# Kernel tuning notes

Hardware: AMD Instinct MI355X
Metric: run time of the kernel (lower is better)

The kernel has to match this reference:

```python
import jax, jax.numpy as jnp
import numpy as np

D_MODEL = 1024
NUM_HEADS = 16
D_HEAD = D_MODEL // NUM_HEADS
NEG_INF = float(np.finfo(np.float32).min)


def setup_inputs() -> dict:
    key = jax.random.key(0)
    ks = jax.random.split(key, 6)
    B, S = 2, 2048
    q = jax.random.normal(ks[0], (B, S, D_MODEL), dtype=jnp.float32)
    k = jax.random.normal(ks[1], (B, S, D_MODEL), dtype=jnp.float32)
    v = jax.random.normal(ks[2], (B, S, D_MODEL), dtype=jnp.float32)
    # causal boolean mask: True = attend
    attn_mask = jnp.tril(jnp.ones((S, S), dtype=bool))
    # nn.Linear(d_model, d_model, bias=False) weights: [out, in]; y = x @ W.T
    init_scale = 1.0 / np.sqrt(D_MODEL)
    Wq = jax.random.uniform(ks[3], (D_MODEL, D_MODEL), jnp.float32, -init_scale, init_scale)
    Wk = jax.random.uniform(ks[4], (D_MODEL, D_MODEL), jnp.float32, -init_scale, init_scale)
    Wv = jax.random.uniform(ks[5], (D_MODEL, D_MODEL), jnp.float32, -init_scale, init_scale)
    return {"query": q, "key": k, "value": v, "Wq": Wq, "Wk": Wk, "Wv": Wv,
            "attn_mask": attn_mask}


def _split_heads(x):
    # [B, S, D_MODEL] -> [B, H, S, d_head]
    B, S, _ = x.shape
    return x.reshape(B, S, NUM_HEADS, D_HEAD).transpose(0, 2, 1, 3)


def reference(query, key, value, Wq, Wk, Wv, attn_mask):
    B, Sq, _ = query.shape
    Sk = key.shape[1]
    q = _split_heads(query @ Wq.T)   # [B, H, Sq, dh]
    k = _split_heads(key @ Wk.T)     # [B, H, Sk, dh]
    v = _split_heads(value @ Wv.T)   # [B, H, Sk, dh]
    scale = 1.0 / np.sqrt(D_HEAD)
    scores = jnp.einsum('bhqd,bhkd->bhqk', q, k) * scale  # [B, H, Sq, Sk]
    scores = jnp.where(attn_mask[None, None, :, :], scores, NEG_INF)
    attn_weights = jax.nn.softmax(scores, axis=-1)
    ctx = jnp.einsum('bhqk,bhkd->bhqd', attn_weights, v)   # [B, H, Sq, dh]
    context = ctx.transpose(0, 2, 1, 3).reshape(B, Sq, D_MODEL)
    return context, attn_weights
```

## Files before the change

### kernel.cpp

```cpp
#include <hip/hip_runtime.h>
#include <hip/hip_bf16.h>

#define B_ 2
#define H_ 16
#define S_ 2048
#define DH_ 64
#define DM_ 1024
#define BH_ (B_*H_)
#define CTX_ELEMS (B_*S_*DM_)
#define ATTNW_ELEMS ((size_t)BH_*S_*S_)
#define HEAD_ELEMS (S_*DH_)

typedef __attribute__((ext_vector_type(4))) float  f32x4;
typedef __attribute__((ext_vector_type(8))) short  short8;
typedef __attribute__((ext_vector_type(4))) unsigned short ush4;
typedef unsigned short u16;
typedef unsigned int u32;

__device__ __forceinline__ u16 f2bf(float f) {
  union { __hip_bfloat16 h; u16 u; } cv;
  cv.h = __float2bfloat16(f);
  return cv.u;
}
__device__ __forceinline__ float bf2f(u16 u) {
  union { unsigned int i; float f; } cv;
  cv.i = ((unsigned int)u) << 16;
  return cv.f;
}

__device__ __forceinline__ void gload_lds16(const u16* g, u16* l) {
  __builtin_amdgcn_global_load_lds(
      (const __attribute__((address_space(1))) u32*)g,
      (__attribute__((address_space(3))) u32*)l, 16, 0, 0);
}

__global__ __launch_bounds__(256) void convert_all(
    const float* __restrict__ q, const float* __restrict__ k, const float* __restrict__ v,
    const float* __restrict__ wq, const float* __restrict__ wk, const float* __restrict__ wv,
    u16* __restrict__ xb, u16* __restrict__ wb)
{
  const int t = blockIdx.y;
  const float* s; u16* d; int nblk;
  if (t < 3) {
    s = (t == 0) ? wq : (t == 1) ? wk : wv;
    d = wb + (size_t)t * (DM_ * DM_);
    nblk = 512;
  } else {
    s = (t == 3) ? q : (t == 4) ? k : v;
    d = xb + (size_t)(t - 3) * ((size_t)B_ * S_ * DM_);
    nblk = 2048;
  }
  if (blockIdx.x >= nblk) return;
  const int i = (blockIdx.x * 256 + threadIdx.x) * 8;
  f32x4 a = *(const f32x4*)(s + i);
  f32x4 b = *(const f32x4*)(s + i + 4);
  short8 p;
#pragma unroll
  for (int j = 0; j < 4; ++j) { p[j] = (short)f2bf(a[j]); p[4 + j] = (short)f2bf(b[j]); }
  *(short8*)(d + i) = p;
}

__global__ __launch_bounds__(256) void proj_gemm(
    const u16* __restrict__ Xb, const u16* __restrict__ Wb,
    u16* __restrict__ O0, u16* __restrict__ O1, u16* __restrict__ O2)
{
  u16* O = (blockIdx.z == 0) ? O0 : (blockIdx.z == 1) ? O1 : O2;
  const u16* A = Xb + (size_t)blockIdx.z * ((size_t)B_ * S_ * DM_);
  const u16* W = Wb + (size_t)blockIdx.z * (DM_ * DM_);

  const int m0 = blockIdx.x * 128;
  const int n0 = blockIdx.y * 128;

  __shared__ u16 As[128 * 32];
  __shared__ u16 Bs[128 * 32];

  const int tid  = threadIdx.x;
  const int lane = tid & 63;
  const int w    = tid >> 6;
  const int wr   = w >> 1, wc = w & 1;
  const int l15  = lane & 15, l4 = lane >> 4;

  f32x4 acc[4][4];
#pragma unroll
  for (int i = 0; i < 4; ++i)
#pragma unroll
    for (int j = 0; j < 4; ++j) acc[i][j] = (f32x4){0.f, 0.f, 0.f, 0.f};

  const int srow = lane >> 2;
  const int scol = (lane & 3) * 8;
  const int ca = w * 2;
  const u16* ga0 = A + (size_t)(m0 + ca * 16 + srow) * DM_ + scol;
  const u16* ga1 = A + (size_t)(m0 + ca * 16 + 16 + srow) * DM_ + scol;
  const u16* gb0 = W + (size_t)(n0 + ca * 16 + srow) * DM_ + scol;
  const u16* gb1 = W + (size_t)(n0 + ca * 16 + 16 + srow) * DM_ + scol;

  for (int kb = 0; kb < DM_ / 32; ++kb) {
    const int k0 = kb * 32;
    gload_lds16(ga0 + k0, &As[ca * 512]);
    gload_lds16(ga1 + k0, &As[ca * 512 + 512]);
    gload_lds16(gb0 + k0, &Bs[ca * 512]);
    gload_lds16(gb1 + k0, &Bs[ca * 512 + 512]);
    __syncthreads();
    short8 af[4], bfr[4];
#pragma unroll
    for (int i = 0; i < 4; ++i)
      af[i] = *(const short8*)&As[(wr * 64 + i * 16 + l15) * 32 + l4 * 8];
#pragma unroll
    for (int j = 0; j < 4; ++j)
      bfr[j] = *(const short8*)&Bs[(wc * 64 + j * 16 + l15) * 32 + l4 * 8];
#pragma unroll
    for (int i = 0; i < 4; ++i)
#pragma unroll
      for (int j = 0; j < 4; ++j)
        acc[i][j] = __builtin_amdgcn_mfma_f32_16x16x32_bf16(af[i], bfr[j], acc[i][j], 0, 0, 0);
    __syncthreads();
  }

#pragma unroll
  for (int i = 0; i < 4; ++i) {
#pragma unroll
    for (int j = 0; j < 4; ++j) {
#pragma unroll
      for (int r = 0; r < 4; ++r) {
        const int grow = m0 + wr * 64 + i * 16 + l4 * 4 + r;
        const int gcol = n0 + wc * 64 + j * 16 + l15;
        const int b = grow >> 11, s = grow & (S_ - 1);
        const int h = gcol >> 6,  d = gcol & (DH_ - 1);
        O[(size_t)((b << 4) + h) * HEAD_ELEMS + (size_t)s * DH_ + d] = f2bf(acc[i][j][r]);
      }
    }
  }
}

__global__ __launch_bounds__(256) void transpose_v(const u16* __restrict__ vb,
                                                   u16* __restrict__ vt)
{
  __shared__ u16 T[64][72];
  const int bh = blockIdx.y;
  const int s0 = blockIdx.x * 64;
  const int tid = threadIdx.x;
  {
    const int sl = tid >> 2, dof = (tid & 3) * 16;
    const u16* src = vb + (size_t)bh * HEAD_ELEMS + (size_t)(s0 + sl) * DH_ + dof;
    *(short8*)&T[sl][dof]     = *(const short8*)(src);
    *(short8*)&T[sl][dof + 8] = *(const short8*)(src + 8);
  }
  __syncthreads();
  {
    const int dd = tid >> 2, sof = (tid & 3) * 16;
    u16* dst = vt + (size_t)bh * HEAD_ELEMS + (size_t)dd * S_ + s0 + sof;
    short8 t0, t1;
#pragma unroll
    for (int j = 0; j < 8; ++j) t0[j] = (short)T[sof + j][dd];
#pragma unroll
    for (int j = 0; j < 8; ++j) t1[j] = (short)T[sof + 8 + j][dd];
    *(short8*)(dst)     = t0;
    *(short8*)(dst + 8) = t1;
  }
}

#define PROW 2048
#define ATT_SMEM (16 * PROW * 2 + 16 * 4 + 64 * 4)

__global__ __launch_bounds__(256) void attn_kernel(
    const u16* __restrict__ qb, const u16* __restrict__ kb, const u16* __restrict__ vt,
    float* __restrict__ ctx, float* __restrict__ attnw)
{
  extern __shared__ u16 smem[];
  u16* P = smem;
  float* rinv    = (float*)(smem + 16 * PROW);
  float* partial = rinv + 16;

  const int lin = blockIdx.y * 128 + blockIdx.x;
  const int nl  = (lin & 7) * 512 + (lin >> 3);
  const int bh  = nl >> 7;
  const int qtl = nl & 127;
  const int qt  = 127 - qtl;

  const int tid = threadIdx.x;
  const int lane = tid & 63;
  const int w = tid >> 6;
  const int l15 = lane & 15, l4 = lane >> 4;

  const int NCC = ((qt * 16 + 16) + 127) >> 7;
  const int ncols = NCC << 7;
  const int qtmax = qt * 16 + 15;

  const u16* Qb = qb + (size_t)bh * HEAD_ELEMS + (size_t)(qt * 16) * DH_;
  const u16* Kb = kb + (size_t)bh * HEAD_ELEMS;
  const u16* Vt = vt + (size_t)bh * HEAD_ELEMS;

  {
    short8 aQ0 = *(const short8*)(Qb + (size_t)l15 * DH_ + l4 * 8);
    short8 aQ1 = *(const short8*)(Qb + (size_t)l15 * DH_ + l4 * 8 + 32);
    const int qrow = l4 * 4;
    const int qabs = qt * 16 + qrow;
    float psum[4] = {0.f, 0.f, 0.f, 0.f};
    for (int ci = 0; ci < NCC; ++ci) {
      const int col0 = (ci << 7) + w * 32;
#pragma unroll
      for (int t = 0; t < 2; ++t) {
        const int ct = col0 + t * 16;
        const int cg = ct + l15;
        if (ct <= qtmax) {
          const u16* kp = Kb + (size_t)cg * DH_ + l4 * 8;
          short8 b0 = *(const short8*)(kp);
          short8 b1 = *(const short8*)(kp + 32);
          f32x4 a0 = (f32x4){0.f, 0.f, 0.f, 0.f};
          f32x4 a1 = (f32x4){0.f, 0.f, 0.f, 0.f};
          a0 = __builtin_amdgcn_mfma_f32_16x16x32_bf16(aQ0, b0, a0, 0, 0, 0);
          a1 = __builtin_amdgcn_mfma_f32_16x16x32_bf16(aQ1, b1, a1, 0, 0, 0);
          const f32x4 a = a0 + a1;
#pragma unroll
          for (int r = 0; r < 4; ++r) {
            const float e = (cg <= qabs + r) ? __expf(a[r] * 0.125f) : 0.f;
            psum[r] += e;
            const int row = qrow + r;
            P[(row << 11) + (cg ^ ((row & 7) << 3))] = f2bf(e);
          }
        } else {
#pragma unroll
          for (int r = 0; r < 4; ++r) {
            const int row = qrow + r;
            P[(row << 11) + (cg ^ ((row & 7) << 3))] = 0;
          }
        }
      }
    }
#pragma unroll
    for (int r = 0; r < 4; ++r) {
      float s = psum[r];
      s += __shfl_xor(s, 1);
      s += __shfl_xor(s, 2);
      s += __shfl_xor(s, 4);
      s += __shfl_xor(s, 8);
      if (l15 == 0) partial[w * 16 + qrow + r] = s;
    }
  }
  __syncthreads();
  if (tid < 16) {
    const float l = partial[tid] + partial[16 + tid] + partial[32 + tid] + partial[48 + tid];
    rinv[tid] = 1.0f / l;
  }
  __syncthreads();

  auto phase2a = [&]() {
    const f32x4 z = (f32x4){0.f, 0.f, 0.f, 0.f};
    const int cl = lane * 4;
#pragma unroll
    for (int rr = 0; rr < 4; ++rr) {
      const int row = w * 4 + rr;
      const float inv = rinv[row];
      const int swz = (row & 7) << 3;
      const u16* prow = P + (row << 11);
      float* orow = attnw + (size_t)bh * ((size_t)S_ * S_) + (size_t)(qt * 16 + row) * S_;
      int c = 0;
      for (; c < ncols; c += 256) {
        const int col = c + cl;
        ush4 pv = *(const ush4*)(prow + (col ^ swz));
        const bool live = col < ncols;
        f32x4 o;
        o[0] = live ? bf2f(pv[0]) * inv : 0.f;
        o[1] = live ? bf2f(pv[1]) * inv : 0.f;
        o[2] = live ? bf2f(pv[2]) * inv : 0.f;
        o[3] = live ? bf2f(pv[3]) * inv : 0.f;
        __builtin_nontemporal_store(o, (f32x4*)(orow + col));
      }
      for (; c < S_; c += 256)
        __builtin_nontemporal_store(z, (f32x4*)(orow + c + cl));
    }
  };

  auto phase2b = [&]() {
    const int dq = w;
    f32x4 acc0 = (f32x4){0.f, 0.f, 0.f, 0.f};
    f32x4 acc1 = (f32x4){0.f, 0.f, 0.f, 0.f};
    const u16* vp0 = Vt + (size_t)(dq * 16 + l15) * S_ + l4 * 8;
    const u16* prow = P + (l15 << 11);
    const int swz = (l15 & 7) << 3;
    for (int c = 0; c < ncols; c += 64) {
      short8 ap0 = *(const short8*)(prow + ((c + l4 * 8) ^ swz));
      short8 bv0 = *(const short8*)(vp0 + c);
      acc0 = __builtin_amdgcn_mfma_f32_16x16x32_bf16(ap0, bv0, acc0, 0, 0, 0);
      short8 ap1 = *(const short8*)(prow + ((c + 32 + l4 * 8) ^ swz));
      short8 bv1 = *(const short8*)(vp0 + c + 32);
      acc1 = __builtin_amdgcn_mfma_f32_16x16x32_bf16(ap1, bv1, acc1, 0, 0, 0);
    }
    const f32x4 acc = acc0 + acc1;
    const int b = bh >> 4, h = bh & 15;
#pragma unroll
    for (int r = 0; r < 4; ++r) {
      const int rg = qt * 16 + l4 * 4 + r;
      const float inv = rinv[l4 * 4 + r];
      ctx[(size_t)(b * S_ + rg) * DM_ + h * 64 + dq * 16 + l15] = acc[r] * inv;
    }
  };

  if (qtl & 1) { phase2b(); phase2a(); }
  else         { phase2a(); phase2b(); }
}

extern "C" void kernel_launch(void* const* d_in, const int* in_sizes, int n_in,
                              void* d_out, int out_size, void* d_ws, size_t ws_size,
                              hipStream_t stream) {
  const float* q  = (const float*)d_in[0];
  const float* k  = (const float*)d_in[1];
  const float* v  = (const float*)d_in[2];
  const float* Wq = (const float*)d_in[3];
  const float* Wk = (const float*)d_in[4];
  const float* Wv = (const float*)d_in[5];

  float* ctx   = (float*)d_out;
  float* attnw = ctx + CTX_ELEMS;

  u16* wb = (u16*)d_ws;
  u16* qb = wb + (size_t)3 * DM_ * DM_;
  u16* kb = qb + (size_t)BH_ * HEAD_ELEMS;
  u16* vb = kb + (size_t)BH_ * HEAD_ELEMS;
  u16* vt = vb + (size_t)BH_ * HEAD_ELEMS;
  u16* xb = (u16*)attnw;

  hipFuncSetAttribute(reinterpret_cast<const void*>(attn_kernel),
                      hipFuncAttributeMaxDynamicSharedMemorySize, ATT_SMEM);

  convert_all<<<dim3(2048, 6), 256, 0, stream>>>(q, k, v, Wq, Wk, Wv, xb, wb);
  proj_gemm<<<dim3(32, 8, 3), 256, 0, stream>>>(xb, wb, qb, kb, vb);
  transpose_v<<<dim3(32, 32), 256, 0, stream>>>(vb, vt);
  attn_kernel<<<dim3(128, 32), 256, ATT_SMEM, stream>>>(qb, kb, vt, ctx, attnw);
}
```

Before: 213.0 us.

## Interleave mirrored-tile zero fill with QK pass and warp-specialize output phase

The zero writes for the masked part of the attention-weight matrix move out of the final phase. Each block now zero-fills the masked columns of its mirrored query tile (index qtl) during the QK/exp loop, so the streaming stores overlap MFMA work. This also pairs long and short zero ranges across blocks. The output phase is split by wave: two waves normalize and write the live attention weights (8 rows each), while the other two compute P·V over two head-dim slices each. This drops the alternating phase order but puts more work on each of the fewer waves per role.

```diff
diff --git a/kernel.cpp b/kernel.cpp
--- a/kernel.cpp
+++ b/kernel.cpp
@@ -190,6 +190,13 @@
   const u16* Kb = kb + (size_t)bh * HEAD_ELEMS;
   const u16* Vt = vt + (size_t)bh * HEAD_ELEMS;
 
+  const int qm = qtl;
+  const int mcols = (((qm * 16 + 16) + 127) >> 7) << 7;
+  float* zbase = attnw + (size_t)bh * ((size_t)S_ * S_) + (size_t)(qm * 16 + w * 4) * S_;
+  const int zro = lane >> 5;
+  const int zcl = (lane & 31) * 4;
+  const f32x4 zv = (f32x4){0.f, 0.f, 0.f, 0.f};
+
   {
     short8 aQ0 = *(const short8*)(Qb + (size_t)l15 * DH_ + l4 * 8);
     short8 aQ1 = *(const short8*)(Qb + (size_t)l15 * DH_ + l4 * 8 + 32);
@@ -197,6 +204,11 @@
     const int qabs = qt * 16 + qrow;
     float psum[4] = {0.f, 0.f, 0.f, 0.f};
     for (int ci = 0; ci < NCC; ++ci) {
+      const int zc = mcols + (ci << 7);
+      if (zc < S_) {
+        __builtin_nontemporal_store(zv, (f32x4*)(zbase + (size_t)zro * S_ + zc + zcl));
+        __builtin_nontemporal_store(zv, (f32x4*)(zbase + (size_t)(2 + zro) * S_ + zc + zcl));
+      }
       const int col0 = (ci << 7) + w * 32;
 #pragma unroll
       for (int t = 0; t < 2; ++t) {
@@ -244,19 +256,15 @@
   }
   __syncthreads();
 
-  auto phase2a = [&]() {
-    const f32x4 z = (f32x4){0.f, 0.f, 0.f, 0.f};
-    const int cl = lane * 4;
-#pragma unroll
-    for (int rr = 0; rr < 4; ++rr) {
-      const int row = w * 4 + rr;
+  if (w < 2) {
+    for (int rr = 0; rr < 8; ++rr) {
+      const int row = w * 8 + rr;
       const float inv = rinv[row];
       const int swz = (row & 7) << 3;
       const u16* prow = P + (row << 11);
       float* orow = attnw + (size_t)bh * ((size_t)S_ * S_) + (size_t)(qt * 16 + row) * S_;
-      int c = 0;
-      for (; c < ncols; c += 256) {
-        const int col = c + cl;
+      for (int c = 0; c < ncols; c += 256) {
+        const int col = c + lane * 4;
         ush4 pv = *(const ush4*)(prow + (col ^ swz));
         const bool live = col < ncols;
         f32x4 o;
@@ -264,40 +272,42 @@
         o[1] = live ? bf2f(pv[1]) * inv : 0.f;
         o[2] = live ? bf2f(pv[2]) * inv : 0.f;
         o[3] = live ? bf2f(pv[3]) * inv : 0.f;
-        __builtin_nontemporal_store(o, (f32x4*)(orow + col));
+        if (live) __builtin_nontemporal_store(o, (f32x4*)(orow + col));
       }
-      for (; c < S_; c += 256)
-        __builtin_nontemporal_store(z, (f32x4*)(orow + c + cl));
-    }
-  };
-
-  auto phase2b = [&]() {
-    const int dq = w;
-    f32x4 acc0 = (f32x4){0.f, 0.f, 0.f, 0.f};
-    f32x4 acc1 = (f32x4){0.f, 0.f, 0.f, 0.f};
-    const u16* vp0 = Vt + (size_t)(dq * 16 + l15) * S_ + l4 * 8;
+    }
+  } else {
+    const int dq0 = (w - 2) * 2;
+    f32x4 a00 = (f32x4){0.f, 0.f, 0.f, 0.f};
+    f32x4 a01 = (f32x4){0.f, 0.f, 0.f, 0.f};
+    f32x4 a10 = (f32x4){0.f, 0.f, 0.f, 0.f};
+    f32x4 a11 = (f32x4){0.f, 0.f, 0.f, 0.f};
+    const u16* vp0 = Vt + (size_t)(dq0 * 16 + l15) * S_ + l4 * 8;
+    const u16* vp1 = vp0 + (size_t)16 * S_;
     const u16* prow = P + (l15 << 11);
     const int swz = (l15 & 7) << 3;
     for (int c = 0; c < ncols; c += 64) {
       short8 ap0 = *(const short8*)(prow + ((c + l4 * 8) ^ swz));
-      short8 bv0 = *(const short8*)(vp0 + c);
-      acc0 = __builtin_amdgcn_mfma_f32_16x16x32_bf16(ap0, bv0, acc0, 0, 0, 0);
       short8 ap1 = *(const short8*)(prow + ((c + 32 + l4 * 8) ^ swz));
-      short8 bv1 = *(const short8*)(vp0 + c + 32);
-      acc1 = __builtin_amdgcn_mfma_f32_16x16x32_bf16(ap1, bv1, acc1, 0, 0, 0);
-    }
-    const f32x4 acc = acc0 + acc1;
+      short8 b00 = *(const short8*)(vp0 + c);
+      short8 b01 = *(const short8*)(vp0 + c + 32);
+      short8 b10 = *(const short8*)(vp1 + c);
+      short8 b11 = *(const short8*)(vp1 + c + 32);
+      a00 = __builtin_amdgcn_mfma_f32_16x16x32_bf16(ap0, b00, a00, 0, 0, 0);
+      a10 = __builtin_amdgcn_mfma_f32_16x16x32_bf16(ap0, b10, a10, 0, 0, 0);
+      a01 = __builtin_amdgcn_mfma_f32_16x16x32_bf16(ap1, b01, a01, 0, 0, 0);
+      a11 = __builtin_amdgcn_mfma_f32_16x16x32_bf16(ap1, b11, a11, 0, 0, 0);
+    }
+    const f32x4 acc0 = a00 + a01;
+    const f32x4 acc1 = a10 + a11;
     const int b = bh >> 4, h = bh & 15;
 #pragma unroll
     for (int r = 0; r < 4; ++r) {
       const int rg = qt * 16 + l4 * 4 + r;
       const float inv = rinv[l4 * 4 + r];
-      ctx[(size_t)(b * S_ + rg) * DM_ + h * 64 + dq * 16 + l15] = acc[r] * inv;
-    }
-  };
-
-  if (qtl & 1) { phase2b(); phase2a(); }
-  else         { phase2a(); phase2b(); }
+      ctx[(size_t)(b * S_ + rg) * DM_ + h * 64 + dq0 * 16 + l15]        = acc0[r] * inv;
+      ctx[(size_t)(b * S_ + rg) * DM_ + h * 64 + (dq0 + 1) * 16 + l15]  = acc1[r] * inv;
+    }
+  }
 }
 
 extern "C" void kernel_launch(void* const* d_in, const int* in_sizes, int n_in,
```

After: 208.4 us. 2.2% less time.

## Warp-specialize attention: extra waves zero-fill mirrored tiles and write attention weights

Applied to the files above, without the earlier changes.

The block doubles to 512 threads. Waves 0-3 compute QK/softmax and then PV, while waves 4-7 first write zeros to the masked tail of a mirrored query tile (qtl instead of qt) and later write the normalized attention weights. This overlaps the large attention-weight stores with MFMA work. The mirrored assignment evens out the zero-fill store volume across blocks, which before was heavy for early query tiles and light for late ones. The cost is higher per-block resource use, which may lower occupancy, and write coverage now relies on the qtl to qt mapping being a bijection.

```diff
diff --git a/kernel.cpp b/kernel.cpp
--- a/kernel.cpp
+++ b/kernel.cpp
@@ -162,7 +162,7 @@
 #define PROW 2048
 #define ATT_SMEM (16 * PROW * 2 + 16 * 4 + 64 * 4)
 
-__global__ __launch_bounds__(256) void attn_kernel(
+__global__ __launch_bounds__(512) void attn_kernel(
     const u16* __restrict__ qb, const u16* __restrict__ kb, const u16* __restrict__ vt,
     float* __restrict__ ctx, float* __restrict__ attnw)
 {
@@ -186,11 +186,12 @@
   const int ncols = NCC << 7;
   const int qtmax = qt * 16 + 15;
 
-  const u16* Qb = qb + (size_t)bh * HEAD_ELEMS + (size_t)(qt * 16) * DH_;
   const u16* Kb = kb + (size_t)bh * HEAD_ELEMS;
   const u16* Vt = vt + (size_t)bh * HEAD_ELEMS;
-
-  {
+  float* attnw_bh = attnw + (size_t)bh * ((size_t)S_ * S_);
+
+  if (w < 4) {
+    const u16* Qb = qb + (size_t)bh * HEAD_ELEMS + (size_t)(qt * 16) * DH_;
     short8 aQ0 = *(const short8*)(Qb + (size_t)l15 * DH_ + l4 * 8);
     short8 aQ1 = *(const short8*)(Qb + (size_t)l15 * DH_ + l4 * 8 + 32);
     const int qrow = l4 * 4;
@@ -236,6 +237,17 @@
       s += __shfl_xor(s, 8);
       if (l15 == 0) partial[w * 16 + qrow + r] = s;
     }
+  } else {
+    const int qm = qtl;
+    const int mcols = (((qm * 16 + 16) + 127) >> 7) << 7;
+    const f32x4 zv = (f32x4){0.f, 0.f, 0.f, 0.f};
+    const int zw = w - 4;
+#pragma unroll
+    for (int rr = 0; rr < 4; ++rr) {
+      float* zrow = attnw_bh + (size_t)(qm * 16 + zw * 4 + rr) * S_;
+      for (int c = mcols + lane * 4; c < S_; c += 256)
+        __builtin_nontemporal_store(zv, (f32x4*)(zrow + c));
+    }
   }
   __syncthreads();
   if (tid < 16) {
@@ -244,34 +256,7 @@
   }
   __syncthreads();
 
-  auto phase2a = [&]() {
-    const f32x4 z = (f32x4){0.f, 0.f, 0.f, 0.f};
-    const int cl = lane * 4;
-#pragma unroll
-    for (int rr = 0; rr < 4; ++rr) {
-      const int row = w * 4 + rr;
-      const float inv = rinv[row];
-      const int swz = (row & 7) << 3;
-      const u16* prow = P + (row << 11);
-      float* orow = attnw + (size_t)bh * ((size_t)S_ * S_) + (size_t)(qt * 16 + row) * S_;
-      int c = 0;
-      for (; c < ncols; c += 256) {
-        const int col = c + cl;
-        ush4 pv = *(const ush4*)(prow + (col ^ swz));
-        const bool live = col < ncols;
-        f32x4 o;
-        o[0] = live ? bf2f(pv[0]) * inv : 0.f;
-        o[1] = live ? bf2f(pv[1]) * inv : 0.f;
-        o[2] = live ? bf2f(pv[2]) * inv : 0.f;
-        o[3] = live ? bf2f(pv[3]) * inv : 0.f;
-        __builtin_nontemporal_store(o, (f32x4*)(orow + col));
-      }
-      for (; c < S_; c += 256)
-        __builtin_nontemporal_store(z, (f32x4*)(orow + c + cl));
-    }
-  };
-
-  auto phase2b = [&]() {
+  if (w < 4) {
     const int dq = w;
     f32x4 acc0 = (f32x4){0.f, 0.f, 0.f, 0.f};
     f32x4 acc1 = (f32x4){0.f, 0.f, 0.f, 0.f};
@@ -294,10 +279,28 @@
       const float inv = rinv[l4 * 4 + r];
       ctx[(size_t)(b * S_ + rg) * DM_ + h * 64 + dq * 16 + l15] = acc[r] * inv;
     }
-  };
-
-  if (qtl & 1) { phase2b(); phase2a(); }
-  else         { phase2a(); phase2b(); }
+  } else {
+    const int sw = w - 4;
+#pragma unroll
+    for (int rr = 0; rr < 4; ++rr) {
+      const int row = sw * 4 + rr;
+      const float inv = rinv[row];
+      const int swz = (row & 7) << 3;
+      const u16* prow = P + (row << 11);
+      float* orow = attnw_bh + (size_t)(qt * 16 + row) * S_;
+      for (int c = 0; c < ncols; c += 256) {
+        const int col = c + lane * 4;
+        ush4 pv = *(const ush4*)(prow + (col ^ swz));
+        const bool live = col < ncols;
+        f32x4 o;
+        o[0] = live ? bf2f(pv[0]) * inv : 0.f;
+        o[1] = live ? bf2f(pv[1]) * inv : 0.f;
+        o[2] = live ? bf2f(pv[2]) * inv : 0.f;
+        o[3] = live ? bf2f(pv[3]) * inv : 0.f;
+        if (live) __builtin_nontemporal_store(o, (f32x4*)(orow + col));
+      }
+    }
+  }
 }
 
 extern "C" void kernel_launch(void* const* d_in, const int* in_sizes, int n_in,
@@ -326,5 +329,5 @@
   convert_all<<<dim3(2048, 6), 256, 0, stream>>>(q, k, v, Wq, Wk, Wv, xb, wb);
   proj_gemm<<<dim3(32, 8, 3), 256, 0, stream>>>(xb, wb, qb, kb, vb);
   transpose_v<<<dim3(32, 32), 256, 0, stream>>>(vb, vt);
-  attn_kernel<<<dim3(128, 32), 256, ATT_SMEM, stream>>>(qb, kb, vt, ctx, attnw);
-}
+  attn_kernel<<<dim3(128, 32), 512, ATT_SMEM, stream>>>(qb, kb, vt, ctx, attnw);
+}
```

New measurement: 216.7 us. Within noise of the previous version (+1.7%).
